# Optimization experiments

Measured on AMD Instinct MI355X. Metric: run time of the kernel, lower is better.

The kernel has to match this reference:

```python
import jax, jax.numpy as jnp
import numpy as np

B, M, N, F, H = 4, 512, 1024, 256, 256
K, K2, KC, RADIUS = 8, 4, 16, 0.5
EPS = 1e-5


def _cdist(a, b):
    d2 = (jnp.sum(a * a, -1)[..., :, None] + jnp.sum(b * b, -1)[..., None, :]
          - 2.0 * jnp.einsum('bnd,bmd->bnm', a, b))
    return jnp.sqrt(jnp.maximum(d2, 0.0))


def _scf_oe(xyz):
    # spherical coords (r, theta, phi) relative to cloud centroid -> (B,3,Npts)
    rel = xyz - jnp.mean(xyz, axis=1, keepdims=True)
    r = jnp.sqrt(jnp.sum(rel * rel, -1) + 1e-8)
    theta = jnp.arccos(jnp.clip(rel[..., 2] / r, -1.0, 1.0))
    phi = jnp.arctan2(rel[..., 1], rel[..., 0])
    return jnp.stack([r, theta, phi], axis=1)


def _knn_desc(xyz):
    # per-point SCF descriptor: sorted distances to KC nearest neighbors
    d = _cdist(xyz, xyz)
    return jnp.sort(d, axis=-1)[..., 1:KC + 1]


def _inorm(x):
    # InstanceNorm1d, affine=False: normalize over last dim per (b, row)
    mu = jnp.mean(x, -1, keepdims=True)
    var = jnp.var(x, -1, keepdims=True)
    return (x - mu) / jnp.sqrt(var + EPS)


def _conv1x1(x, W, g, b):
    # Conv2d 1x1 + BN(affine) + ReLU on (B,C,N,K)
    y = jnp.einsum('bcnk,oc->bonk', x, W)
    return jax.nn.relu(g[:, None, None] * y + b[:, None, None])


def _conv12(x, W, g, b):
    # Conv2d kernel (1,2) stride (1,2) + BN(affine) + ReLU on (B,C,N,P)
    Bb, C, Nn, P = x.shape
    xr = x.reshape(Bb, C, Nn, P // 2, 2)
    y = jnp.einsum('bcnpt,oct->bonp', xr, W)
    return jax.nn.relu(g[:, None, None] * y + b[:, None, None])


def _pointsift(xyz, feat, params):
    # PointSIFT OE: nearest neighbor in each of 8 octants within radius
    w1, g1, b1, w2, g2, b2, w3, g3, b3 = params
    Bb, Nn, _ = xyz.shape
    diff = xyz[:, None, :, :] - xyz[:, :, None, :]  # diff[b,i,j] = xyz[j]-xyz[i]
    d2 = jnp.sum(diff * diff, -1)
    octant = ((diff[..., 0] > 0).astype(jnp.int32) * 4
              + (diff[..., 1] > 0).astype(jnp.int32) * 2
              + (diff[..., 2] > 0).astype(jnp.int32))
    base = jnp.broadcast_to(jnp.arange(Nn)[None, :], (Bb, Nn))
    idxs = []
    for c in range(8):  # fixed small structural loop
        m = (octant == c) & (d2 <= RADIUS * RADIUS) & (d2 > 0)
        dm = jnp.where(m, d2, jnp.inf)
        j = jnp.argmin(dm, -1)
        valid = jnp.isfinite(jnp.min(dm, -1))
        idxs.append(jnp.where(valid, j, base))
    idx = jnp.stack(idxs, -1)  # (B,N,8)
    gxyz = jax.vmap(lambda p, i: p[i])(xyz, idx) - xyz[:, :, None, :]
    gfeat = jax.vmap(lambda f, i: f[i])(feat, idx)
    g = jnp.concatenate([gxyz, gfeat], -1).transpose(0, 3, 1, 2)  # (B,3+C,N,8)
    g = _conv12(g, w1, g1, b1)
    g = _conv12(g, w2, g2, b2)
    g = _conv12(g, w3, g3, b3)
    return g[..., 0]  # (B,C,N)


def setup_inputs():
    key = jax.random.key(0)
    ks = iter(jax.random.split(key, 64))
    rn = lambda shape, s=0.05: jax.random.normal(next(ks), shape, dtype=jnp.float32) * s
    ones = lambda shape: jnp.ones(shape, jnp.float32)
    zeros = lambda shape: jnp.zeros(shape, jnp.float32)
    inp = {
        'template_feature': rn((B, F, M), 1.0),
        'search_feature': rn((B, F, N), 1.0),
        'template_xyz': rn((B, M, 3), 1.0),
        'search_xyz': rn((B, N, 3), 1.0),
        'template_bc': rn((B, M, 9), 1.0),
        'search_bc': rn((B, N, 9), 1.0),
        'mlp_w1': rn((H, F + 3)), 'mlp_g1': ones(H), 'mlp_b1': zeros(H),
        'mlp_w2': rn((H, H)), 'mlp_g2': ones(H), 'mlp_b2': zeros(H),
        'mlp_w3': rn((H, H)), 'mlp_g3': ones(H), 'mlp_b3': zeros(H),
        'fea_w1': rn((F, H)), 'fea_g1': ones(F), 'fea_b1': zeros(F),
        'fea_w2': rn((F, F)), 'fea_bias2': zeros(F),
        'attn_wqkv': rn((3 * F, F)),
        'pos_w1': rn((64, 12)), 'pos_b1': zeros(64),
        'pos_w2': rn((F, 64)), 'pos_b2': zeros(F),
        'amlp_w1': rn((4 * F, F)), 'amlp_b1': zeros(4 * F),
        'amlp_w2': rn((F, 4 * F)), 'amlp_b2': zeros(F),
        'oe1_w1': rn((F, F + 3, 2)), 'oe1_g1': ones(F), 'oe1_b1': zeros(F),
        'oe1_w2': rn((F, F, 2)), 'oe1_g2': ones(F), 'oe1_b2': zeros(F),
        'oe1_w3': rn((F, F, 2)), 'oe1_g3': ones(F), 'oe1_b3': zeros(F),
        'oe2_w1': rn((F, F + 3, 2)), 'oe2_g1': ones(F), 'oe2_b1': zeros(F),
        'oe2_w2': rn((F, F, 2)), 'oe2_g2': ones(F), 'oe2_b2': zeros(F),
        'oe2_w3': rn((F, F, 2)), 'oe2_g3': ones(F), 'oe2_b3': zeros(F),
    }
    return inp


def reference(template_feature, search_feature, template_xyz, search_xyz, template_bc, search_bc,
              mlp_w1, mlp_g1, mlp_b1, mlp_w2, mlp_g2, mlp_b2, mlp_w3, mlp_g3, mlp_b3,
              fea_w1, fea_g1, fea_b1, fea_w2, fea_bias2,
              attn_wqkv, pos_w1, pos_b1, pos_w2, pos_b2, amlp_w1, amlp_b1, amlp_w2, amlp_b2,
              oe1_w1, oe1_g1, oe1_b1, oe1_w2, oe1_g2, oe1_b2, oe1_w3, oe1_g3, oe1_b3,
              oe2_w1, oe2_g1, oe2_b1, oe2_w2, oe2_g2, oe2_b2, oe2_w3, oe2_g3, oe2_b3):
    # ---- box-cloud distance + candidate pruning ----
    dist_bc = _cdist(template_bc, search_bc)  # (B,M,N)
    t_box = jnp.concatenate([template_xyz.transpose(0, 2, 1), template_bc.transpose(0, 2, 1),
                             template_feature, _scf_oe(template_xyz)], 1)  # (B,15+F,M)
    s_box = jnp.concatenate([search_xyz.transpose(0, 2, 1), search_bc.transpose(0, 2, 1),
                             search_feature, _scf_oe(search_xyz)], 1)      # (B,15+F,N)
    idx_b = jnp.argsort(dist_bc, axis=1)[:, :3 * K, :].transpose(0, 2, 1)  # (B,N,3K)
    dist_xyz = _cdist(search_xyz, template_xyz)  # (B,N,M)
    bi = jnp.arange(B)[:, None, None]
    ni = jnp.arange(N)[None, :, None]
    mask = jnp.full((B, N, M), 1e5, jnp.float32).at[bi, ni, idx_b].set(1.0)
    idx_k = jnp.argsort((dist_xyz * mask).transpose(0, 2, 1), axis=1)[:, :K, :].transpose(0, 2, 1)  # (B,N,K)
    # ---- SCF descriptor matching restricted to xyz candidates ----
    sd = _knn_desc(search_xyz)
    td = _knn_desc(template_xyz)
    mask2 = jnp.full((B, N, M), 1e5, jnp.float32).at[bi, ni, idx_k].set(1.0)
    dist_scf = _cdist(sd, td) * mask2
    idx_s = jnp.argsort(dist_scf.transpose(0, 2, 1), axis=1)[:, :K2, :].transpose(0, 2, 1)  # (B,N,K2)
    # ---- grouping + shared MLP ----
    corr = jax.vmap(lambda f, i: f[:, i])(t_box, idx_s)        # (B,15+F,N,K2)
    fused = jnp.concatenate([s_box[..., None], corr], -1)      # (B,15+F,N,K2+1)
    feats = fused.transpose(0, 2, 3, 1)[..., 12:]              # drop xyz+bc -> (B,N,K2+1,F+3)
    h = feats.transpose(0, 3, 1, 2)
    h = _conv1x1(h, mlp_w1, mlp_g1, mlp_b1)
    h = _conv1x1(h, mlp_w2, mlp_g2, mlp_b2)
    h = _conv1x1(h, mlp_w3, mlp_g3, mlp_b3)
    h = h.transpose(0, 2, 3, 1)                                # (B,N,K2+1,H)
    nn_xyz = corr[:, 0:3].transpose(0, 2, 3, 1)
    st_xyz = jnp.concatenate([search_xyz[:, :, None, :], nn_xyz], 2)
    nn_bc = corr[:, 3:12].transpose(0, 2, 3, 1)
    st_bc = jnp.concatenate([search_bc[:, :, None, :], nn_bc], 2)
    pos = jnp.concatenate([st_xyz, st_bc], -1)                 # (B,N,K2+1,12)
    KP1 = K2 + 1
    x = h.reshape(B * N, KP1, H)
    p = pos.reshape(B * N, KP1, 12)
    # ---- point transformer layer over tiny neighborhoods ----
    qkv = jnp.einsum('bnd,ed->bne', x, attn_wqkv)
    q, k, v = jnp.split(qkv, 3, axis=-1)
    rel_pos = p[:, :, None, :] - p[:, None, :, :]
    pe = jnp.einsum('bijp,hp->bijh', rel_pos, pos_w1) + pos_b1
    pe = jnp.einsum('bijh,dh->bijd', jax.nn.relu(pe), pos_w2) + pos_b2
    sim_in = q[:, :, None, :] - k[:, None, :, :] + pe
    hh = jax.nn.relu(jnp.einsum('bijd,hd->bijh', sim_in, amlp_w1) + amlp_b1)
    sim = jnp.einsum('bijh,dh->bijd', hh, amlp_w2) + amlp_b2
    attn = jax.nn.softmax(sim, axis=-2)
    agg = jnp.einsum('bijd,bijd->bid', attn, v[:, None, :, :] + pe)
    ff = agg.reshape(B, N, KP1, H).transpose(0, 3, 1, 2)[..., 0]  # (B,F,N)
    # ---- residual + instance norms + fea_layer ----
    ff = ff + search_feature
    ff = _inorm(ff.transpose(0, 2, 1)).transpose(0, 2, 1)
    y = jax.nn.relu(fea_g1[:, None] * jnp.einsum('bcn,oc->bon', ff, fea_w1) + fea_b1[:, None])
    y = jnp.einsum('bcn,oc->bon', y, fea_w2) + fea_bias2[:, None]
    y = _inorm((y + ff).transpose(0, 2, 1)).transpose(0, 2, 1)
    # ---- two PointSIFT OE modules with residuals ----
    y = y + _pointsift(search_xyz, y.transpose(0, 2, 1), (oe1_w1, oe1_g1, oe1_b1, oe1_w2, oe1_g2, oe1_b2, oe1_w3, oe1_g3, oe1_b3))
    y = y + _pointsift(search_xyz, y.transpose(0, 2, 1), (oe2_w1, oe2_g1, oe2_b1, oe2_w2, oe2_g2, oe2_b2, oe2_w3, oe2_g3, oe2_b3))
    return y
```

## Files before the change

### kernel.cpp

```cpp
#include <hip/hip_runtime.h>
#include <hip/hip_bf16.h>
#include <math.h>

constexpr int Bc = 4, Mc = 512, Nc = 1024, Fc = 256;
constexpr int KCc = 16;
constexpr float INFF = 3.0e38f;

typedef __attribute__((ext_vector_type(8))) short short8b;
typedef __attribute__((ext_vector_type(4))) float f32x4;

__device__ __forceinline__ short f2bf(float f) {
  __hip_bfloat16 h = __float2bfloat16(f);
  return *reinterpret_cast<short*>(&h);
}
__device__ __forceinline__ float bf2f(short s) {
  unsigned int u = ((unsigned int)(unsigned short)s) << 16;
  return __uint_as_float(u);
}
__device__ __forceinline__ unsigned long long umin64(unsigned long long a, unsigned long long b) {
  return a < b ? a : b;
}

__device__ __forceinline__ float blk_sum(float v, float* red) {
  int t = threadIdx.x;
// ... 34 lines not shown
    v = (k < 256) ? s.p[5][(size_t)(512 + r) * 256 + k] : pw2[(size_t)r * 64 + (k - 256)];
  else
    v = (k < K) ? s.p[job][(size_t)r * K + k] : 0.f;
  dstbase[gi] = f2bf(v);
}

__global__ __launch_bounds__(256) void scf_kernel(const float* __restrict__ xyz,
                                                  float* __restrict__ out, int P) {
  __shared__ float red[256];
  int b = blockIdx.x;
  const float* x = xyz + (size_t)b * P * 3;
  float sx = 0.f, sy = 0.f, sz = 0.f;
  for (int i = threadIdx.x; i < P; i += 256) {
    sx += x[3 * i]; sy += x[3 * i + 1]; sz += x[3 * i + 2];
  }
  float mx = blk_sum(sx, red) / (float)P;
  float my = blk_sum(sy, red) / (float)P;
  float mz = blk_sum(sz, red) / (float)P;
  for (int i = threadIdx.x; i < P; i += 256) {
    float a = x[3 * i] - mx, c = x[3 * i + 1] - my, d = x[3 * i + 2] - mz;
    float r = sqrtf(a * a + c * c + d * d + 1e-8f);
    float ct = d / r;
    ct = fminf(1.f, fmaxf(-1.f, ct));
    out[((size_t)b * 3 + 0) * P + i] = r;
    out[((size_t)b * 3 + 1) * P + i] = acosf(ct);
    out[((size_t)b * 3 + 2) * P + i] = atan2f(c, a);
  }
}

template <int P>
__global__ __launch_bounds__(256) void knn_kernel(const float* __restrict__ xyz,
                                                  float* __restrict__ desc) {
  constexpr int E = P / 64;
  int wv = threadIdx.x >> 6, l = threadIdx.x & 63;
  int pt = blockIdx.x * 4 + wv;
  int b = pt / P, i = pt % P;
  const float* x = xyz + (size_t)b * P * 3;
  float xi0 = x[3 * i], xi1 = x[3 * i + 1], xi2 = x[3 * i + 2];
  float d2r[E];
#pragma unroll
  for (int q = 0; q < E; ++q) {
    int j = q * 64 + l;
    float dx = x[3 * j] - xi0, dy = x[3 * j + 1] - xi1, dz = x[3 * j + 2] - xi2;
    d2r[q] = dx * dx + dy * dy + dz * dz;
  }
  for (int round = 0; round < KCc + 1; ++round) {
    unsigned long long k = ~0ULL;
#pragma unroll
    for (int q = 0; q < E; ++q) {
      unsigned long long c =
          ((unsigned long long)__float_as_uint(d2r[q]) << 32) | (unsigned)(q * 64 + l);
      k = umin64(k, c);
    }
#pragma unroll
    for (int m = 1; m < 64; m <<= 1) k = umin64(k, __shfl_xor(k, m));
    int widx = (int)(unsigned)k;
    if (round > 0 && l == 0)
      desc[((size_t)b * P + i) * KCc + (round - 1)] = sqrtf(__uint_as_float((unsigned)(k >> 32)));
    if ((widx & 63) == l) {
      int q = widx >> 6;
#pragma unroll
      for (int qq = 0; qq < E; ++qq)
        if (qq == q) d2r[qq] = INFF;
    }
  }
}

__global__ __launch_bounds__(256) void select_kernel(
    const float* __restrict__ tbc, const float* __restrict__ sbc,
    const float* __restrict__ txyz, const float* __restrict__ sxyz,
    const float* __restrict__ sd, const float* __restrict__ td,
    int* __restrict__ idx_s) {
  __shared__ int cand4[4][24];
  int wv = threadIdx.x >> 6, l = threadIdx.x & 63;
  int pt = blockIdx.x * 4 + wv;
  int b = pt / Nc, n = pt % Nc;
  const float* sb = sbc + ((size_t)b * Nc + n) * 9;
  float sreg[9];
#pragma unroll
  for (int c = 0; c < 9; ++c) sreg[c] = sb[c];
  float d2r[8];
#pragma unroll
  for (int q = 0; q < 8; ++q) {
    int m = q * 64 + l;
    const float* tb = tbc + ((size_t)b * Mc + m) * 9;
    float acc = 0.f;
#pragma unroll
    for (int c = 0; c < 9; ++c) { float d = tb[c] - sreg[c]; acc += d * d; }
    d2r[q] = acc;
  }
  for (int round = 0; round < 24; ++round) {
    unsigned long long k = ~0ULL;
#pragma unroll
    for (int q = 0; q < 8; ++q) {
      unsigned long long c =
          ((unsigned long long)__float_as_uint(d2r[q]) << 32) | (unsigned)(q * 64 + l);
      k = umin64(k, c);
    }
#pragma unroll
    for (int m = 1; m < 64; m <<= 1) k = umin64(k, __shfl_xor(k, m));
    int widx = (int)(unsigned)k;
    if (l == 0) cand4[wv][round] = widx;
    if ((widx & 63) == l) {
      int q = widx >> 6;
#pragma unroll
      for (int qq = 0; qq < 8; ++qq)
        if (qq == q) d2r[qq] = INFF;
    }
  }
  if (l == 0) {
    int* cand = cand4[wv];
    const float* sp = sxyz + ((size_t)b * Nc + n) * 3;
    float sx = sp[0], sy = sp[1], sz = sp[2];
    float dv[24];
    for (int t2 = 0; t2 < 24; ++t2) {
      const float* tp = txyz + ((size_t)b * Mc + cand[t2]) * 3;
      float dx = tp[0] - sx, dy = tp[1] - sy, dz = tp[2] - sz;
      dv[t2] = dx * dx + dy * dy + dz * dz;
    }
    int c8[8]; bool used[24];
    for (int t2 = 0; t2 < 24; ++t2) used[t2] = false;
    for (int r = 0; r < 8; ++r) {
      float bv = INFF; int bt = -1, bm = 0x7fffffff;
      for (int t2 = 0; t2 < 24; ++t2) {
        if (used[t2]) continue;
        int m = cand[t2];
        if (bt < 0 || dv[t2] < bv || (dv[t2] == bv && m < bm)) { bv = dv[t2]; bt = t2; bm = m; }
      }
      used[bt] = true; c8[r] = bm;
    }
    const float* sdp = sd + ((size_t)b * Nc + n) * KCc;
    float sdr[16];
    for (int t2 = 0; t2 < 16; ++t2) sdr[t2] = sdp[t2];
    float dscf[8];
    for (int r = 0; r < 8; ++r) {
      const float* tdp = td + ((size_t)b * Mc + c8[r]) * KCc;
      float acc = 0.f;
      for (int t2 = 0; t2 < 16; ++t2) { float d = sdr[t2] - tdp[t2]; acc += d * d; }
      dscf[r] = acc;
    }
    bool u8[8] = {false, false, false, false, false, false, false, false};
    for (int r = 0; r < 4; ++r) {
      float bv = INFF; int bt = -1, bm = 0x7fffffff;
      for (int t2 = 0; t2 < 8; ++t2) {
        if (u8[t2]) continue;
        if (bt < 0 || dscf[t2] < bv || (dscf[t2] == bv && c8[t2] < bm)) { bv = dscf[t2]; bt = t2; bm = c8[t2]; }
      }
      u8[bt] = true;
      idx_s[(((size_t)b * Nc + n) << 2) + r] = bm;
    }
  }
}

__global__ __launch_bounds__(512, 4) void mlp_kernel(
    const float* __restrict__ sfeat, const float* __restrict__ tfeat,
    const float* __restrict__ sscf, const float* __restrict__ tscf,
    const int* __restrict__ idx_s,
    const short* __restrict__ w1f, const float* __restrict__ g1, const float* __restrict__ b1,
    const short* __restrict__ w2f, const float* __restrict__ g2, const float* __restrict__ b2,
    const short* __restrict__ w3f, const float* __restrict__ g3, const float* __restrict__ b3,
    short* __restrict__ houtS) {
  __shared__ __align__(16) char smem[52224];
  char* B1 = smem;
  char* B2 = smem + 27648;
  char* B3 = smem;
  __shared__ int ms[32];
  int t = threadIdx.x;
  int tau0 = blockIdx.x * 8;
  int b = tau0 / Nc, n0 = tau0 % Nc;
  int h = t >> 8, ch = t & 255;
  if (t < 32) ms[t] = idx_s[(((size_t)b * Nc + n0 + (t >> 2)) << 2) + (t & 3)];
  __syncthreads();
  for (int z = t; z < 48 * 29; z += 512) {
    int col = z / 29, k = 259 + z % 29;
    *(short*)(B1 + ((col * 576 + 2 * k) ^ ((col & 7) << 4))) = 0;
  }
  for (int z = t; z < 8 * 259; z += 512) {
    int col = 40 + z / 259, k = z % 259;
    *(short*)(B1 + ((col * 576 + 2 * k) ^ ((col & 7) << 4))) = 0;
  }
  for (int sj = h; sj < 40; sj += 2) {
    int s = sj / 5, j = sj % 5;
    int n = n0 + s;
    int cx = (sj & 7) << 4;
    if (j == 0) {
      *(short*)(B1 + ((sj * 576 + 2 * ch) ^ cx)) = f2bf(sfeat[((size_t)b * Fc + ch) * Nc + n]);
      if (ch < 3)
        *(short*)(B1 + ((sj * 576 + (256 + ch) * 2) ^ cx)) = f2bf(sscf[((size_t)b * 3 + ch) * Nc + n]);
    } else {
      int m = ms[s * 4 + j - 1];
      *(short*)(B1 + ((sj * 576 + 2 * ch) ^ cx)) = f2bf(tfeat[((size_t)b * Fc + ch) * Mc + m]);
      if (ch < 3)
        *(short*)(B1 + ((sj * 576 + (256 + ch) * 2) ^ cx)) = f2bf(tscf[((size_t)b * 3 + ch) * Mc + m]);
    }
  }
  __syncthreads();
  int l = t & 63, w = t >> 6, lg = l >> 4, lr = l & 15;
  {
    f32x4 acc[2][3];
#pragma unroll
    for (int i = 0; i < 2; ++i)
#pragma unroll
      for (int ct = 0; ct < 3; ++ct) acc[i][ct] = (f32x4){0,0,0,0};
    for (int kk = 0; kk < 9; ++kk) {
      short8b bb[3];
#pragma unroll
      for (int ct = 0; ct < 3; ++ct) {
        int col = ct * 16 + lr;
        bb[ct] = *(const short8b*)(B1 + ((col * 576 + kk * 64 + lg * 16) ^ ((col & 7) << 4)));
      }
#pragma unroll
      for (int i = 0; i < 2; ++i) {
        short8b a = *(const short8b*)(w1f + (((size_t)((w * 2 + i) * 9 + kk)) * 64 + l) * 8);
#pragma unroll
        for (int ct = 0; ct < 3; ++ct)
          acc[i][ct] = __builtin_amdgcn_mfma_f32_16x16x32_bf16(a, bb[ct], acc[i][ct], 0, 0, 0);
      }
    }
    __syncthreads();
#pragma unroll
    for (int i = 0; i < 2; ++i) {
      int r0 = (w * 2 + i) * 16 + lg * 4;
      float4 gg = *(const float4*)(g1 + r0), bs = *(const float4*)(b1 + r0);
#pragma unroll
      for (int ct = 0; ct < 3; ++ct) {
        int col = ct * 16 + lr; int cx = (col & 7) << 4;
        ushort4 hv;
        hv.x = (unsigned short)f2bf(fmaxf(gg.x * acc[i][ct][0] + bs.x, 0.f));
        hv.y = (unsigned short)f2bf(fmaxf(gg.y * acc[i][ct][1] + bs.y, 0.f));
        hv.z = (unsigned short)f2bf(fmaxf(gg.z * acc[i][ct][2] + bs.z, 0.f));
        hv.w = (unsigned short)f2bf(fmaxf(gg.w * acc[i][ct][3] + bs.w, 0.f));
        *(ushort4*)(B2 + ((col * 512 + r0 * 2) ^ cx)) = hv;
      }
    }
  }
  __syncthreads();
  {
    f32x4 acc[2][3];
#pragma unroll
    for (int i = 0; i < 2; ++i)
#pragma unroll
      for (int ct = 0; ct < 3; ++ct) acc[i][ct] = (f32x4){0,0,0,0};
    for (int kk = 0; kk < 8; ++kk) {
      short8b bb[3];
#pragma unroll
      for (int ct = 0; ct < 3; ++ct) {
        int col = ct * 16 + lr;
        bb[ct] = *(const short8b*)(B2 + ((col * 512 + kk * 64 + lg * 16) ^ ((col & 7) << 4)));
      }
#pragma unroll
      for (int i = 0; i < 2; ++i) {
        short8b a = *(const short8b*)(w2f + (((size_t)((w * 2 + i) * 8 + kk)) * 64 + l) * 8);
#pragma unroll
        for (int ct = 0; ct < 3; ++ct)
          acc[i][ct] = __builtin_amdgcn_mfma_f32_16x16x32_bf16(a, bb[ct], acc[i][ct], 0, 0, 0);
      }
    }
    __syncthreads();
#pragma unroll
    for (int i = 0; i < 2; ++i) {
      int r0 = (w * 2 + i) * 16 + lg * 4;
      float4 gg = *(const float4*)(g2 + r0), bs = *(const float4*)(b2 + r0);
#pragma unroll
      for (int ct = 0; ct < 3; ++ct) {
        int col = ct * 16 + lr; int cx = (col & 7) << 4;
        ushort4 hv;
        hv.x = (unsigned short)f2bf(fmaxf(gg.x * acc[i][ct][0] + bs.x, 0.f));
        hv.y = (unsigned short)f2bf(fmaxf(gg.y * acc[i][ct][1] + bs.y, 0.f));
        hv.z = (unsigned short)f2bf(fmaxf(gg.z * acc[i][ct][2] + bs.z, 0.f));
        hv.w = (unsigned short)f2bf(fmaxf(gg.w * acc[i][ct][3] + bs.w, 0.f));
        *(ushort4*)(B3 + ((col * 512 + r0 * 2) ^ cx)) = hv;
      }
    }
  }
  __syncthreads();
  {
    f32x4 acc[2][3];
#pragma unroll
    for (int i = 0; i < 2; ++i)
#pragma unroll
      for (int ct = 0; ct < 3; ++ct) acc[i][ct] = (f32x4){0,0,0,0};
    for (int kk = 0; kk < 8; ++kk) {
      short8b bb[3];
#pragma unroll
      for (int ct = 0; ct < 3; ++ct) {
        int col = ct * 16 + lr;
        bb[ct] = *(const short8b*)(B3 + ((col * 512 + kk * 64 + lg * 16) ^ ((col & 7) << 4)));
      }
#pragma unroll
      for (int i = 0; i < 2; ++i) {
        short8b a = *(const short8b*)(w3f + (((size_t)((w * 2 + i) * 8 + kk)) * 64 + l) * 8);
#pragma unroll
        for (int ct = 0; ct < 3; ++ct)
          acc[i][ct] = __builtin_amdgcn_mfma_f32_16x16x32_bf16(a, bb[ct], acc[i][ct], 0, 0, 0);
      }
    }
#pragma unroll
    for (int i = 0; i < 2; ++i) {
      int r0 = (w * 2 + i) * 16 + lg * 4;
      float4 gg = *(const float4*)(g3 + r0), bs = *(const float4*)(b3 + r0);
#pragma unroll
      for (int ct = 0; ct < 3; ++ct) {
        int col = ct * 16 + lr;
        if (col < 40) {
          ushort4 hv;
          hv.x = (unsigned short)f2bf(fmaxf(gg.x * acc[i][ct][0] + bs.x, 0.f));
          hv.y = (unsigned short)f2bf(fmaxf(gg.y * acc[i][ct][1] + bs.y, 0.f));
          hv.z = (unsigned short)f2bf(fmaxf(gg.z * acc[i][ct][2] + bs.z, 0.f));
          hv.w = (unsigned short)f2bf(fmaxf(gg.w * acc[i][ct][3] + bs.w, 0.f));
          int s = col / 5, j = col % 5;
          *(ushort4*)(houtS + ((size_t)(tau0 + s) * 5 + j) * 256 + r0) = hv;
        }
      }
    }
  }
}

__global__ __launch_bounds__(512, 4) void attn_kernel(
    const short* __restrict__ hbufS, const int* __restrict__ idx_s,
    const float* __restrict__ sxyz, const float* __restrict__ sbc,
    const float* __restrict__ txyz, const float* __restrict__ tbc,
    const short* __restrict__ aqf, const short* __restrict__ akpef, const short* __restrict__ avpef,
    const float* __restrict__ pw1, const float* __restrict__ pb1, const float* __restrict__ pb2,
    const short* __restrict__ aw1f, const float* __restrict__ ab1,
    const short* __restrict__ aw2f, const float* __restrict__ ab2,
    const float* __restrict__ sfeat,
    const short* __restrict__ fw1f, const float* __restrict__ fg1, const float* __restrict__ fb1,
    const short* __restrict__ fw2f, const float* __restrict__ fb2v,
    float* __restrict__ yout) {
  __shared__ __align__(16) char smem[79872];
  char* Bx   = smem;
  char* vpeB = smem;
  char* feaB = smem;
  char* feaH = smem + 8192;
  float* y2F = (float*)(smem + 16384);
  char* KB   = smem + 30720;
  char* simS = smem + 30720;
  char* HpB  = smem + 55296;
  float* qF  = (float*)(smem + 55296);
  float* q04 = (float*)(smem + 55296);
  float* redf = (float*)(smem + 63488);
  float* pc4 = (float*)(smem + 64000);
  int t = threadIdx.x;
  int tau0 = blockIdx.x * 8;
  int b = tau0 / Nc, n0 = tau0 % Nc;
  int w = t >> 6, l = t & 63, lg = l >> 4, lr = l & 15;
  int h = t >> 8, ch = t & 255;
  for (int z = t; z < 2560; z += 512) {
    int col = 40 + z / 320, k = z % 320;
    *(short*)(Bx + ((col * 640 + 2 * k) ^ ((col & 7) << 4))) = 0;
  }
  for (int sj = h; sj < 40; sj += 2) {
    int s = sj / 5, j = sj % 5;
    *(short*)(Bx + ((sj * 640 + 2 * ch) ^ ((sj & 7) << 4))) =
        hbufS[(size_t)(tau0 + s) * 1280 + j * 256 + ch];
  }
  if (t < 40) {
    int s = t / 5, k = t % 5;
    int n = n0 + s;
    float* pd = pc4 + t * 12;
    if (k == 0) {
      for (int c = 0; c < 3; ++c) pd[c] = sxyz[((size_t)b * Nc + n) * 3 + c];
      for (int c = 0; c < 9; ++c) pd[3 + c] = sbc[((size_t)b * Nc + n) * 9 + c];
    } else {
      int m = idx_s[(((size_t)b * Nc + n) << 2) + (k - 1)];
      for (int c = 0; c < 3; ++c) pd[c] = txyz[((size_t)b * Mc + m) * 3 + c];
      for (int c = 0; c < 9; ++c) pd[3 + c] = tbc[((size_t)b * Mc + m) * 9 + c];
    }
  }
  __syncthreads();
  for (int it = t; it < 2560; it += 512) {
    int sj = it >> 6, hh = it & 63;
    int s = sj / 5;
    float acc = pb1[hh];
    const float* wv = pw1 + hh * 12;
    const float* p0 = pc4 + (s * 5) * 12;
    const float* pj = pc4 + sj * 12;
#pragma unroll
    for (int p = 0; p < 12; ++p) acc += wv[p] * (p0[p] - pj[p]);
    *(short*)(Bx + ((sj * 640 + 512 + 2 * hh) ^ ((sj & 7) << 4))) = f2bf(fmaxf(acc, 0.f));
  }
  __syncthreads();
  {
    f32x4 qA[2][3];
#pragma unroll
    for (int i = 0; i < 2; ++i)
#pragma unroll
      for (int ct = 0; ct < 3; ++ct) qA[i][ct] = (f32x4){0,0,0,0};
    for (int kk = 0; kk < 8; ++kk) {
      short8b bq[3];
#pragma unroll
      for (int ct = 0; ct < 3; ++ct) {
        int col = ct * 16 + lr;
        bq[ct] = *(const short8b*)(Bx + ((col * 640 + kk * 64 + lg * 16) ^ ((col & 7) << 4)));
      }
#pragma unroll
      for (int i = 0; i < 2; ++i) {
        short8b a = *(const short8b*)(aqf + (((size_t)((w * 2 + i) * 8 + kk)) * 64 + l) * 8);
#pragma unroll
        for (int ct = 0; ct < 3; ++ct)
          qA[i][ct] = __builtin_amdgcn_mfma_f32_16x16x32_bf16(a, bq[ct], qA[i][ct], 0, 0, 0);
      }
    }
#pragma unroll
    for (int i = 0; i < 2; ++i) {
      int r0 = (w * 2 + i) * 16 + lg * 4;
#pragma unroll
      for (int ct = 0; ct < 3; ++ct) {
        int col = ct * 16 + lr;
        if (col < 40 && col % 5 == 0)
          *(f32x4*)(qF + (col / 5) * 256 + r0) = qA[i][ct];
      }
    }
  }
  f32x4 sA[2][3], vA[2][3];
#pragma unroll
  for (int i = 0; i < 2; ++i)
#pragma unroll
    for (int ct = 0; ct < 3; ++ct) { sA[i][ct] = (f32x4){0,0,0,0}; vA[i][ct] = (f32x4){0,0,0,0}; }
  for (int kk = 0; kk < 10; ++kk) {
    short8b bb[3];
#pragma unroll
    for (int ct = 0; ct < 3; ++ct) {
      int col = ct * 16 + lr;
      bb[ct] = *(const short8b*)(Bx + ((col * 640 + kk * 64 + lg * 16) ^ ((col & 7) << 4)));
    }
#pragma unroll
    for (int i = 0; i < 2; ++i) {
      short8b ak = *(const short8b*)(akpef + (((size_t)((w * 2 + i) * 10 + kk)) * 64 + l) * 8);
      short8b av = *(const short8b*)(avpef + (((size_t)((w * 2 + i) * 10 + kk)) * 64 + l) * 8);
#pragma unroll
      for (int ct = 0; ct < 3; ++ct) {
        sA[i][ct] = __builtin_amdgcn_mfma_f32_16x16x32_bf16(ak, bb[ct], sA[i][ct], 0, 0, 0);
        vA[i][ct] = __builtin_amdgcn_mfma_f32_16x16x32_bf16(av, bb[ct], vA[i][ct], 0, 0, 0);
      }
    }
  }
  __syncthreads();
#pragma unroll
  for (int i = 0; i < 2; ++i) {
    int r0 = (w * 2 + i) * 16 + lg * 4;
    float4 pb = *(const float4*)(pb2 + r0);
#pragma unroll
    for (int ct = 0; ct < 3; ++ct) {
      int col = ct * 16 + lr; int cx = (col & 7) << 4;
      if (col < 40) {
        int s = col / 5;
        f32x4 qv = *(const f32x4*)(qF + s * 256 + r0);
        ushort4 kv, vv;
        kv.x = (unsigned short)f2bf(qv[0] + sA[i][ct][0] + pb.x);
        kv.y = (unsigned short)f2bf(qv[1] + sA[i][ct][1] + pb.y);
        kv.z = (unsigned short)f2bf(qv[2] + sA[i][ct][2] + pb.z);
        kv.w = (unsigned short)f2bf(qv[3] + sA[i][ct][3] + pb.w);
        vv.x = (unsigned short)f2bf(vA[i][ct][0] + pb.x);
        vv.y = (unsigned short)f2bf(vA[i][ct][1] + pb.y);
        vv.z = (unsigned short)f2bf(vA[i][ct][2] + pb.z);
        vv.w = (unsigned short)f2bf(vA[i][ct][3] + pb.w);
        *(ushort4*)(KB + ((col * 512 + r0 * 2) ^ cx)) = kv;
        *(ushort4*)(vpeB + ((col * 512 + r0 * 2) ^ cx)) = vv;
      } else {
        ushort4 zz; zz.x = zz.y = zz.z = zz.w = 0;
        *(ushort4*)(KB + ((col * 512 + r0 * 2) ^ cx)) = zz;
      }
    }
  }
  __syncthreads();
  f32x4 sacc[2][3];
#pragma unroll
  for (int i = 0; i < 2; ++i)
#pragma unroll
    for (int ct = 0; ct < 3; ++ct) sacc[i][ct] = (f32x4){0,0,0,0};
  for (int p = 0; p < 4; ++p) {
    f32x4 hacc[2][3];
#pragma unroll
    for (int i = 0; i < 2; ++i)
#pragma unroll
      for (int ct = 0; ct < 3; ++ct) hacc[i][ct] = (f32x4){0,0,0,0};
    for (int kk = 0; kk < 8; ++kk) {
      short8b bb[3];
#pragma unroll
      for (int ct = 0; ct < 3; ++ct) {
        int col = ct * 16 + lr;
        bb[ct] = *(const short8b*)(KB + ((col * 512 + kk * 64 + lg * 16) ^ ((col & 7) << 4)));
      }
#pragma unroll
      for (int i = 0; i < 2; ++i) {
        int rtg = p * 16 + w * 2 + i;
        short8b a = *(const short8b*)(aw1f + (((size_t)(rtg * 8 + kk)) * 64 + l) * 8);
#pragma unroll
        for (int ct = 0; ct < 3; ++ct)
          hacc[i][ct] = __builtin_amdgcn_mfma_f32_16x16x32_bf16(a, bb[ct], hacc[i][ct], 0, 0, 0);
      }
    }
#pragma unroll
    for (int i = 0; i < 2; ++i) {
      int r0l = (w * 2 + i) * 16 + lg * 4;
      float4 bias = *(const float4*)(ab1 + p * 256 + r0l);
#pragma unroll
      for (int ct = 0; ct < 3; ++ct) {
        int col = ct * 16 + lr; int cx = (col & 7) << 4;
        ushort4 hv;
        hv.x = (unsigned short)f2bf(fmaxf(hacc[i][ct][0] + bias.x, 0.f));
        hv.y = (unsigned short)f2bf(fmaxf(hacc[i][ct][1] + bias.y, 0.f));
        hv.z = (unsigned short)f2bf(fmaxf(hacc[i][ct][2] + bias.z, 0.f));
        hv.w = (unsigned short)f2bf(fmaxf(hacc[i][ct][3] + bias.w, 0.f));
        *(ushort4*)(HpB + ((col * 512 + r0l * 2) ^ cx)) = hv;
      }
    }
    __syncthreads();
// ... 291 lines not shown
        *(short*)(B2 + ((col2 * 1024 + (2 * (r0 + 1) + tp) * 2) ^ cx2)) =
            f2bf(fmaxf(gg.y * acc[i][ct][1] + bs.y, 0.f));
        *(short*)(B2 + ((col2 * 1024 + (2 * (r0 + 2) + tp) * 2) ^ cx2)) =
            f2bf(fmaxf(gg.z * acc[i][ct][2] + bs.z, 0.f));
        *(short*)(B2 + ((col2 * 1024 + (2 * (r0 + 3) + tp) * 2) ^ cx2)) =
            f2bf(fmaxf(gg.w * acc[i][ct][3] + bs.w, 0.f));
      }
    }
  }
  __syncthreads();
  {
    f32x4 acc[2];
#pragma unroll
    for (int i = 0; i < 2; ++i) acc[i] = (f32x4){0,0,0,0};
    for (int kk = 0; kk < 16; ++kk) {
      short8b b0 = *(const short8b*)(B2 + ((lr * 1024 + kk * 64 + lg * 16) ^ ((lr & 7) << 4)));
#pragma unroll
      for (int i = 0; i < 2; ++i) {
        short8b a = *(const short8b*)(w2f + (((size_t)((w * 2 + i) * 16 + kk)) * 64 + l) * 8);
        acc[i] = __builtin_amdgcn_mfma_f32_16x16x32_bf16(a, b0, acc[i], 0, 0, 0);
      }
    }
    __syncthreads();
    int s = lr >> 1, tp = lr & 1;
    int col3 = s; int cx3 = (col3 & 7) << 4;
#pragma unroll
    for (int i = 0; i < 2; ++i) {
      int r0 = (w * 2 + i) * 16 + lg * 4;
      float4 gg = *(const float4*)(g2 + r0), bs = *(const float4*)(b2 + r0);
      *(short*)(B3 + ((col3 * 1024 + (2 * r0 + tp) * 2) ^ cx3)) =
          f2bf(fmaxf(gg.x * acc[i][0] + bs.x, 0.f));
      *(short*)(B3 + ((col3 * 1024 + (2 * (r0 + 1) + tp) * 2) ^ cx3)) =
          f2bf(fmaxf(gg.y * acc[i][1] + bs.y, 0.f));
      *(short*)(B3 + ((col3 * 1024 + (2 * (r0 + 2) + tp) * 2) ^ cx3)) =
          f2bf(fmaxf(gg.z * acc[i][2] + bs.z, 0.f));
      *(short*)(B3 + ((col3 * 1024 + (2 * (r0 + 3) + tp) * 2) ^ cx3)) =
          f2bf(fmaxf(gg.w * acc[i][3] + bs.w, 0.f));
    }
  }
  __syncthreads();
  {
    f32x4 acc[2];
#pragma unroll
    for (int i = 0; i < 2; ++i) acc[i] = (f32x4){0,0,0,0};
    for (int kk = 0; kk < 16; ++kk) {
      short8b b0 = *(const short8b*)(B3 + ((lr * 1024 + kk * 64 + lg * 16) ^ ((lr & 7) << 4)));
#pragma unroll
      for (int i = 0; i < 2; ++i) {
        short8b a = *(const short8b*)(w3f + (((size_t)((w * 2 + i) * 16 + kk)) * 64 + l) * 8);
        acc[i] = __builtin_amdgcn_mfma_f32_16x16x32_bf16(a, b0, acc[i], 0, 0, 0);
      }
    }
#pragma unroll
    for (int i = 0; i < 2; ++i) {
      if (lr < 8) {
        int s = lr;
        int r0 = (w * 2 + i) * 16 + lg * 4;
        float4 gg = *(const float4*)(g3 + r0), bs = *(const float4*)(b3 + r0);
        float4 yv = *(const float4*)(yin + ((size_t)(i0 + s)) * 256 + r0);
        float4 ov;
        ov.x = yv.x + fmaxf(gg.x * acc[i][0] + bs.x, 0.f);
        ov.y = yv.y + fmaxf(gg.y * acc[i][1] + bs.y, 0.f);
        ov.z = yv.z + fmaxf(gg.z * acc[i][2] + bs.z, 0.f);
        ov.w = yv.w + fmaxf(gg.w * acc[i][3] + bs.w, 0.f);
        *(float4*)(yout + ((size_t)(i0 + s)) * 256 + r0) = ov;
      }
    }
  }
}

__global__ __launch_bounds__(256) void transpose_kernel(const float* __restrict__ yin,
                                                        float* __restrict__ out) {
  __shared__ float tile[64][65];
  int bid = blockIdx.x;
  int b = bid >> 6;
  int tl = bid & 63;
  int n0 = (tl >> 2) * 64;
  int c0 = (tl & 3) * 64;
  int tx = threadIdx.x & 63, ty = threadIdx.x >> 6;
#pragma unroll
  for (int r = 0; r < 16; ++r) {
    int i = r * 4 + ty;
    tile[i][tx] = yin[((size_t)b * Nc + n0 + i) * 256 + c0 + tx];
  }
  __syncthreads();
#pragma unroll
  for (int r = 0; r < 16; ++r) {
    int j = r * 4 + ty;
    out[((size_t)b * Fc + c0 + j) * Nc + n0 + tx] = tile[tx][j];
  }
}

extern "C" void kernel_launch(void* const* d_in, const int* in_sizes, int n_in,
                              void* d_out, int out_size, void* d_ws, size_t ws_size,
                              hipStream_t stream) {
  (void)in_sizes; (void)n_in; (void)out_size; (void)ws_size;
  const float* tfeat = (const float*)d_in[0];
  const float* sfeat = (const float*)d_in[1];
  const float* txyz  = (const float*)d_in[2];
  const float* sxyz  = (const float*)d_in[3];
  const float* tbc   = (const float*)d_in[4];
  const float* sbc   = (const float*)d_in[5];
  const float* mw1 = (const float*)d_in[6];
  const float* mg1 = (const float*)d_in[7];
  const float* mb1 = (const float*)d_in[8];
  const float* mw2 = (const float*)d_in[9];
  const float* mg2 = (const float*)d_in[10];
  const float* mb2 = (const float*)d_in[11];
  const float* mw3 = (const float*)d_in[12];
  const float* mg3 = (const float*)d_in[13];
  const float* mb3 = (const float*)d_in[14];
  const float* fw1 = (const float*)d_in[15];
  const float* fg1 = (const float*)d_in[16];
  const float* fb1 = (const float*)d_in[17];
  const float* fw2 = (const float*)d_in[18];
  const float* fb2 = (const float*)d_in[19];
  const float* wqkv = (const float*)d_in[20];
  const float* pw1 = (const float*)d_in[21];
  const float* pb1 = (const float*)d_in[22];
  const float* pw2 = (const float*)d_in[23];
  const float* pb2 = (const float*)d_in[24];
  const float* aw1 = (const float*)d_in[25];
  const float* ab1 = (const float*)d_in[26];
  const float* aw2 = (const float*)d_in[27];
  const float* ab2 = (const float*)d_in[28];
  const float* o1w1 = (const float*)d_in[29];
  const float* o1g1 = (const float*)d_in[30];
  const float* o1b1 = (const float*)d_in[31];
  const float* o1w2 = (const float*)d_in[32];
  const float* o1g2 = (const float*)d_in[33];
  const float* o1b2 = (const float*)d_in[34];
  const float* o1w3 = (const float*)d_in[35];
  const float* o1g3 = (const float*)d_in[36];
  const float* o1b3 = (const float*)d_in[37];
  const float* o2w1 = (const float*)d_in[38];
  const float* o2g1 = (const float*)d_in[39];
  const float* o2b1 = (const float*)d_in[40];
  const float* o2w2 = (const float*)d_in[41];
  const float* o2g2 = (const float*)d_in[42];
  const float* o2b2 = (const float*)d_in[43];
  const float* o2w3 = (const float*)d_in[44];
  const float* o2g3 = (const float*)d_in[45];
  const float* o2b3 = (const float*)d_in[46];

  float* ws = (float*)d_ws;
  float* sd   = ws;
  float* td   = sd + 65536;
  float* sscf = td + 32768;
  float* tscf = sscf + 12288;
  int*   idxs = (int*)(tscf + 6144);
  int*   sidx = idxs + 16384;
  float* yws  = (float*)(sidx + 32768);
  short* sb   = (short*)(yws + 1048576);
  short* hbufS = sb;
  short* mw1f  = sb + 5242880;
  short* mw2f  = mw1f + 73728;
  short* mw3f  = mw2f + 65536;
  short* aqf   = mw3f + 65536;
  short* akpef = aqf + 65536;
  short* avpef = akpef + 81920;
  short* aw1f  = avpef + 81920;
  short* aw2f  = aw1f + 262144;
  short* fw1f  = aw2f + 262144;
  short* fw2f  = fw1f + 65536;
  short* o1w1f = fw2f + 65536;
  short* o1w2f = o1w1f + 139264;
  short* o1w3f = o1w2f + 131072;
  short* o2w1f = o1w3f + 131072;
  short* o2w2f = o2w1f + 139264;
  short* o2w3f = o2w2f + 131072;
  float* ybuf2 = (float*)sb;

  WSrcs srcs;
  srcs.p[0] = mw1;  srcs.p[1] = mw2;  srcs.p[2] = mw3;  srcs.p[3] = wqkv;
  srcs.p[4] = wqkv; srcs.p[5] = wqkv; srcs.p[6] = aw1;  srcs.p[7] = aw2;
  srcs.p[8] = fw1;  srcs.p[9] = fw2;  srcs.p[10] = o1w1; srcs.p[11] = o1w2;
  srcs.p[12] = o1w3; srcs.p[13] = o2w1; srcs.p[14] = o2w2; srcs.p[15] = o2w3;
  wconv_all<<<7392, 256, 0, stream>>>(srcs, pw2, mw1f);

  scf_kernel<<<Bc, 256, 0, stream>>>(sxyz, sscf, Nc);
  scf_kernel<<<Bc, 256, 0, stream>>>(txyz, tscf, Mc);
  knn_kernel<Nc><<<Bc * Nc / 4, 256, 0, stream>>>(sxyz, sd);
  knn_kernel<Mc><<<Bc * Mc / 4, 256, 0, stream>>>(txyz, td);
  select_kernel<<<Bc * Nc / 4, 256, 0, stream>>>(tbc, sbc, txyz, sxyz, sd, td, idxs);
  mlp_kernel<<<Bc * Nc / 8, 512, 0, stream>>>(sfeat, tfeat, sscf, tscf, idxs,
                                              mw1f, mg1, mb1, mw2f, mg2, mb2,
                                              mw3f, mg3, mb3, hbufS);
  attn_kernel<<<Bc * Nc / 8, 512, 0, stream>>>(hbufS, idxs, sxyz, sbc, txyz, tbc,
                                               aqf, akpef, avpef, pw1, pb1, pb2,
                                               aw1f, ab1, aw2f, ab2,
                                               sfeat, fw1f, fg1, fb1, fw2f, fb2, yws);
  sift_idx_kernel<<<Bc * Nc / 4, 256, 0, stream>>>(sxyz, sidx);
  sift_oe_kernel<<<Bc * Nc / 8, 512, 0, stream>>>(sxyz, sidx, yws,
                                                  o1w1f, o1g1, o1b1, o1w2f, o1g2, o1b2,
                                                  o1w3f, o1g3, o1b3, ybuf2);
  sift_oe_kernel<<<Bc * Nc / 8, 512, 0, stream>>>(sxyz, sidx, ybuf2,
                                                  o2w1f, o2g1, o2b1, o2w2f, o2g2, o2b2,
                                                  o2w3f, o2g3, o2b3, yws);
  transpose_kernel<<<256, 256, 0, stream>>>(yws, (float*)d_out);
}
```

Baseline: 315.9 us.

## Fuse MLP stage into attention kernel, keeping hidden features in LDS

Merges the three-layer MLP kernel into the attention kernel so the per-point hidden features go straight from the MLP epilogue into the attention input buffer in shared memory. This drops the global round-trip of the bf16 hidden buffer and one kernel launch. MLP buffers are placed in distinct LDS regions, with an extra barrier, so the final layer can write into the attention layout. The fused kernel keeps the larger 78KB LDS footprint for the whole run, which may limit occupancy during the MLP phase.

```diff
diff --git a/kernel.cpp b/kernel.cpp
--- a/kernel.cpp
+++ b/kernel.cpp
@@ -210,183 +210,26 @@
   }
 }
 
-__global__ __launch_bounds__(512, 4) void mlp_kernel(
+__global__ __launch_bounds__(512, 4) void mlp_attn_kernel(
     const float* __restrict__ sfeat, const float* __restrict__ tfeat,
     const float* __restrict__ sscf, const float* __restrict__ tscf,
     const int* __restrict__ idx_s,
-    const short* __restrict__ w1f, const float* __restrict__ g1, const float* __restrict__ b1,
-    const short* __restrict__ w2f, const float* __restrict__ g2, const float* __restrict__ b2,
-    const short* __restrict__ w3f, const float* __restrict__ g3, const float* __restrict__ b3,
-    short* __restrict__ houtS) {
-  __shared__ __align__(16) char smem[52224];
-  char* B1 = smem;
-  char* B2 = smem + 27648;
-  char* B3 = smem;
-  __shared__ int ms[32];
-  int t = threadIdx.x;
-  int tau0 = blockIdx.x * 8;
-  int b = tau0 / Nc, n0 = tau0 % Nc;
-  int h = t >> 8, ch = t & 255;
-  if (t < 32) ms[t] = idx_s[(((size_t)b * Nc + n0 + (t >> 2)) << 2) + (t & 3)];
-  __syncthreads();
-  for (int z = t; z < 48 * 29; z += 512) {
-    int col = z / 29, k = 259 + z % 29;
-    *(short*)(B1 + ((col * 576 + 2 * k) ^ ((col & 7) << 4))) = 0;
-  }
-  for (int z = t; z < 8 * 259; z += 512) {
-    int col = 40 + z / 259, k = z % 259;
-    *(short*)(B1 + ((col * 576 + 2 * k) ^ ((col & 7) << 4))) = 0;
-  }
-  for (int sj = h; sj < 40; sj += 2) {
-    int s = sj / 5, j = sj % 5;
-    int n = n0 + s;
-    int cx = (sj & 7) << 4;
-    if (j == 0) {
-      *(short*)(B1 + ((sj * 576 + 2 * ch) ^ cx)) = f2bf(sfeat[((size_t)b * Fc + ch) * Nc + n]);
-      if (ch < 3)
-        *(short*)(B1 + ((sj * 576 + (256 + ch) * 2) ^ cx)) = f2bf(sscf[((size_t)b * 3 + ch) * Nc + n]);
-    } else {
-      int m = ms[s * 4 + j - 1];
-      *(short*)(B1 + ((sj * 576 + 2 * ch) ^ cx)) = f2bf(tfeat[((size_t)b * Fc + ch) * Mc + m]);
-      if (ch < 3)
-        *(short*)(B1 + ((sj * 576 + (256 + ch) * 2) ^ cx)) = f2bf(tscf[((size_t)b * 3 + ch) * Mc + m]);
-    }
-  }
-  __syncthreads();
-  int l = t & 63, w = t >> 6, lg = l >> 4, lr = l & 15;
-  {
-    f32x4 acc[2][3];
-#pragma unroll
-    for (int i = 0; i < 2; ++i)
-#pragma unroll
-      for (int ct = 0; ct < 3; ++ct) acc[i][ct] = (f32x4){0,0,0,0};
-    for (int kk = 0; kk < 9; ++kk) {
-      short8b bb[3];
-#pragma unroll
-      for (int ct = 0; ct < 3; ++ct) {
-        int col = ct * 16 + lr;
-        bb[ct] = *(const short8b*)(B1 + ((col * 576 + kk * 64 + lg * 16) ^ ((col & 7) << 4)));
-      }
-#pragma unroll
-      for (int i = 0; i < 2; ++i) {
-        short8b a = *(const short8b*)(w1f + (((size_t)((w * 2 + i) * 9 + kk)) * 64 + l) * 8);
-#pragma unroll
-        for (int ct = 0; ct < 3; ++ct)
-          acc[i][ct] = __builtin_amdgcn_mfma_f32_16x16x32_bf16(a, bb[ct], acc[i][ct], 0, 0, 0);
-      }
-    }
-    __syncthreads();
-#pragma unroll
-    for (int i = 0; i < 2; ++i) {
-      int r0 = (w * 2 + i) * 16 + lg * 4;
-      float4 gg = *(const float4*)(g1 + r0), bs = *(const float4*)(b1 + r0);
-#pragma unroll
-      for (int ct = 0; ct < 3; ++ct) {
-        int col = ct * 16 + lr; int cx = (col & 7) << 4;
-        ushort4 hv;
-        hv.x = (unsigned short)f2bf(fmaxf(gg.x * acc[i][ct][0] + bs.x, 0.f));
-        hv.y = (unsigned short)f2bf(fmaxf(gg.y * acc[i][ct][1] + bs.y, 0.f));
-        hv.z = (unsigned short)f2bf(fmaxf(gg.z * acc[i][ct][2] + bs.z, 0.f));
-        hv.w = (unsigned short)f2bf(fmaxf(gg.w * acc[i][ct][3] + bs.w, 0.f));
-        *(ushort4*)(B2 + ((col * 512 + r0 * 2) ^ cx)) = hv;
-      }
-    }
-  }
-  __syncthreads();
-  {
-    f32x4 acc[2][3];
-#pragma unroll
-    for (int i = 0; i < 2; ++i)
-#pragma unroll
-      for (int ct = 0; ct < 3; ++ct) acc[i][ct] = (f32x4){0,0,0,0};
-    for (int kk = 0; kk < 8; ++kk) {
-      short8b bb[3];
-#pragma unroll
-      for (int ct = 0; ct < 3; ++ct) {
-        int col = ct * 16 + lr;
-        bb[ct] = *(const short8b*)(B2 + ((col * 512 + kk * 64 + lg * 16) ^ ((col & 7) << 4)));
-      }
-#pragma unroll
-      for (int i = 0; i < 2; ++i) {
-        short8b a = *(const short8b*)(w2f + (((size_t)((w * 2 + i) * 8 + kk)) * 64 + l) * 8);
-#pragma unroll
-        for (int ct = 0; ct < 3; ++ct)
-          acc[i][ct] = __builtin_amdgcn_mfma_f32_16x16x32_bf16(a, bb[ct], acc[i][ct], 0, 0, 0);
-      }
-    }
-    __syncthreads();
-#pragma unroll
-    for (int i = 0; i < 2; ++i) {
-      int r0 = (w * 2 + i) * 16 + lg * 4;
-      float4 gg = *(const float4*)(g2 + r0), bs = *(const float4*)(b2 + r0);
-#pragma unroll
-      for (int ct = 0; ct < 3; ++ct) {
-        int col = ct * 16 + lr; int cx = (col & 7) << 4;
-        ushort4 hv;
-        hv.x = (unsigned short)f2bf(fmaxf(gg.x * acc[i][ct][0] + bs.x, 0.f));
-        hv.y = (unsigned short)f2bf(fmaxf(gg.y * acc[i][ct][1] + bs.y, 0.f));
-        hv.z = (unsigned short)f2bf(fmaxf(gg.z * acc[i][ct][2] + bs.z, 0.f));
-        hv.w = (unsigned short)f2bf(fmaxf(gg.w * acc[i][ct][3] + bs.w, 0.f));
-        *(ushort4*)(B3 + ((col * 512 + r0 * 2) ^ cx)) = hv;
-      }
-    }
-  }
-  __syncthreads();
-  {
-    f32x4 acc[2][3];
-#pragma unroll
-    for (int i = 0; i < 2; ++i)
-#pragma unroll
-      for (int ct = 0; ct < 3; ++ct) acc[i][ct] = (f32x4){0,0,0,0};
-    for (int kk = 0; kk < 8; ++kk) {
-      short8b bb[3];
-#pragma unroll
-      for (int ct = 0; ct < 3; ++ct) {
-        int col = ct * 16 + lr;
-        bb[ct] = *(const short8b*)(B3 + ((col * 512 + kk * 64 + lg * 16) ^ ((col & 7) << 4)));
-      }
-#pragma unroll
-      for (int i = 0; i < 2; ++i) {
-        short8b a = *(const short8b*)(w3f + (((size_t)((w * 2 + i) * 8 + kk)) * 64 + l) * 8);
-#pragma unroll
-        for (int ct = 0; ct < 3; ++ct)
-          acc[i][ct] = __builtin_amdgcn_mfma_f32_16x16x32_bf16(a, bb[ct], acc[i][ct], 0, 0, 0);
-      }
-    }
-#pragma unroll
-    for (int i = 0; i < 2; ++i) {
-      int r0 = (w * 2 + i) * 16 + lg * 4;
-      float4 gg = *(const float4*)(g3 + r0), bs = *(const float4*)(b3 + r0);
-#pragma unroll
-      for (int ct = 0; ct < 3; ++ct) {
-        int col = ct * 16 + lr;
-        if (col < 40) {
-          ushort4 hv;
-          hv.x = (unsigned short)f2bf(fmaxf(gg.x * acc[i][ct][0] + bs.x, 0.f));
-          hv.y = (unsigned short)f2bf(fmaxf(gg.y * acc[i][ct][1] + bs.y, 0.f));
-          hv.z = (unsigned short)f2bf(fmaxf(gg.z * acc[i][ct][2] + bs.z, 0.f));
-          hv.w = (unsigned short)f2bf(fmaxf(gg.w * acc[i][ct][3] + bs.w, 0.f));
-          int s = col / 5, j = col % 5;
-          *(ushort4*)(houtS + ((size_t)(tau0 + s) * 5 + j) * 256 + r0) = hv;
-        }
-      }
-    }
-  }
-}
-
-__global__ __launch_bounds__(512, 4) void attn_kernel(
-    const short* __restrict__ hbufS, const int* __restrict__ idx_s,
+    const short* __restrict__ mw1f, const float* __restrict__ mg1, const float* __restrict__ mb1,
+    const short* __restrict__ mw2f, const float* __restrict__ mg2, const float* __restrict__ mb2,
+    const short* __restrict__ mw3f, const float* __restrict__ mg3, const float* __restrict__ mb3,
     const float* __restrict__ sxyz, const float* __restrict__ sbc,
     const float* __restrict__ txyz, const float* __restrict__ tbc,
     const short* __restrict__ aqf, const short* __restrict__ akpef, const short* __restrict__ avpef,
     const float* __restrict__ pw1, const float* __restrict__ pb1, const float* __restrict__ pb2,
     const short* __restrict__ aw1f, const float* __restrict__ ab1,
     const short* __restrict__ aw2f, const float* __restrict__ ab2,
-    const float* __restrict__ sfeat,
     const short* __restrict__ fw1f, const float* __restrict__ fg1, const float* __restrict__ fb1,
     const short* __restrict__ fw2f, const float* __restrict__ fb2v,
     float* __restrict__ yout) {
   __shared__ __align__(16) char smem[79872];
+  char* mB1 = smem;
+  char* mB2 = smem + 27648;
+  char* mB3 = smem + 52224;
   char* Bx   = smem;
   char* vpeB = smem;
   char* feaB = smem;
@@ -399,20 +242,162 @@
   float* q04 = (float*)(smem + 55296);
   float* redf = (float*)(smem + 63488);
   float* pc4 = (float*)(smem + 64000);
+  __shared__ int ms[32];
   int t = threadIdx.x;
   int tau0 = blockIdx.x * 8;
   int b = tau0 / Nc, n0 = tau0 % Nc;
   int w = t >> 6, l = t & 63, lg = l >> 4, lr = l & 15;
   int h = t >> 8, ch = t & 255;
-  for (int z = t; z < 2560; z += 512) {
-    int col = 40 + z / 320, k = z % 320;
-    *(short*)(Bx + ((col * 640 + 2 * k) ^ ((col & 7) << 4))) = 0;
+  if (t < 32) ms[t] = idx_s[(((size_t)b * Nc + n0 + (t >> 2)) << 2) + (t & 3)];
+  __syncthreads();
+  for (int z = t; z < 48 * 29; z += 512) {
+    int col = z / 29, k = 259 + z % 29;
+    *(short*)(mB1 + ((col * 576 + 2 * k) ^ ((col & 7) << 4))) = 0;
+  }
+  for (int z = t; z < 8 * 259; z += 512) {
+    int col = 40 + z / 259, k = z % 259;
+    *(short*)(mB1 + ((col * 576 + 2 * k) ^ ((col & 7) << 4))) = 0;
   }
   for (int sj = h; sj < 40; sj += 2) {
     int s = sj / 5, j = sj % 5;
-    *(short*)(Bx + ((sj * 640 + 2 * ch) ^ ((sj & 7) << 4))) =
-        hbufS[(size_t)(tau0 + s) * 1280 + j * 256 + ch];
-  }
+    int n = n0 + s;
+    int cx = (sj & 7) << 4;
+    if (j == 0) {
+      *(short*)(mB1 + ((sj * 576 + 2 * ch) ^ cx)) = f2bf(sfeat[((size_t)b * Fc + ch) * Nc + n]);
+      if (ch < 3)
+        *(short*)(mB1 + ((sj * 576 + (256 + ch) * 2) ^ cx)) = f2bf(sscf[((size_t)b * 3 + ch) * Nc + n]);
+    } else {
+      int m = ms[s * 4 + j - 1];
+      *(short*)(mB1 + ((sj * 576 + 2 * ch) ^ cx)) = f2bf(tfeat[((size_t)b * Fc + ch) * Mc + m]);
+      if (ch < 3)
+        *(short*)(mB1 + ((sj * 576 + (256 + ch) * 2) ^ cx)) = f2bf(tscf[((size_t)b * 3 + ch) * Mc + m]);
+    }
+  }
+  __syncthreads();
+  {
+    f32x4 acc[2][3];
+#pragma unroll
+    for (int i = 0; i < 2; ++i)
+#pragma unroll
+      for (int ct = 0; ct < 3; ++ct) acc[i][ct] = (f32x4){0,0,0,0};
+    for (int kk = 0; kk < 9; ++kk) {
+      short8b bb[3];
+#pragma unroll
+      for (int ct = 0; ct < 3; ++ct) {
+        int col = ct * 16 + lr;
+        bb[ct] = *(const short8b*)(mB1 + ((col * 576 + kk * 64 + lg * 16) ^ ((col & 7) << 4)));
+      }
+#pragma unroll
+      for (int i = 0; i < 2; ++i) {
+        short8b a = *(const short8b*)(mw1f + (((size_t)((w * 2 + i) * 9 + kk)) * 64 + l) * 8);
+#pragma unroll
+        for (int ct = 0; ct < 3; ++ct)
+          acc[i][ct] = __builtin_amdgcn_mfma_f32_16x16x32_bf16(a, bb[ct], acc[i][ct], 0, 0, 0);
+      }
+    }
+    __syncthreads();
+#pragma unroll
+    for (int i = 0; i < 2; ++i) {
+      int r0 = (w * 2 + i) * 16 + lg * 4;
+      float4 gg = *(const float4*)(mg1 + r0), bs = *(const float4*)(mb1 + r0);
+#pragma unroll
+      for (int ct = 0; ct < 3; ++ct) {
+        int col = ct * 16 + lr; int cx = (col & 7) << 4;
+        ushort4 hv;
+        hv.x = (unsigned short)f2bf(fmaxf(gg.x * acc[i][ct][0] + bs.x, 0.f));
+        hv.y = (unsigned short)f2bf(fmaxf(gg.y * acc[i][ct][1] + bs.y, 0.f));
+        hv.z = (unsigned short)f2bf(fmaxf(gg.z * acc[i][ct][2] + bs.z, 0.f));
+        hv.w = (unsigned short)f2bf(fmaxf(gg.w * acc[i][ct][3] + bs.w, 0.f));
+        *(ushort4*)(mB2 + ((col * 512 + r0 * 2) ^ cx)) = hv;
+      }
+    }
+  }
+  __syncthreads();
+  {
+    f32x4 acc[2][3];
+#pragma unroll
+    for (int i = 0; i < 2; ++i)
+#pragma unroll
+      for (int ct = 0; ct < 3; ++ct) acc[i][ct] = (f32x4){0,0,0,0};
+    for (int kk = 0; kk < 8; ++kk) {
+      short8b bb[3];
+#pragma unroll
+      for (int ct = 0; ct < 3; ++ct) {
+        int col = ct * 16 + lr;
+        bb[ct] = *(const short8b*)(mB2 + ((col * 512 + kk * 64 + lg * 16) ^ ((col & 7) << 4)));
+      }
+#pragma unroll
+      for (int i = 0; i < 2; ++i) {
+        short8b a = *(const short8b*)(mw2f + (((size_t)((w * 2 + i) * 8 + kk)) * 64 + l) * 8);
+#pragma unroll
+        for (int ct = 0; ct < 3; ++ct)
+          acc[i][ct] = __builtin_amdgcn_mfma_f32_16x16x32_bf16(a, bb[ct], acc[i][ct], 0, 0, 0);
+      }
+    }
+    __syncthreads();
+#pragma unroll
+    for (int i = 0; i < 2; ++i) {
+      int r0 = (w * 2 + i) * 16 + lg * 4;
+      float4 gg = *(const float4*)(mg2 + r0), bs = *(const float4*)(mb2 + r0);
+#pragma unroll
+      for (int ct = 0; ct < 3; ++ct) {
+        int col = ct * 16 + lr; int cx = (col & 7) << 4;
+        ushort4 hv;
+        hv.x = (unsigned short)f2bf(fmaxf(gg.x * acc[i][ct][0] + bs.x, 0.f));
+        hv.y = (unsigned short)f2bf(fmaxf(gg.y * acc[i][ct][1] + bs.y, 0.f));
+        hv.z = (unsigned short)f2bf(fmaxf(gg.z * acc[i][ct][2] + bs.z, 0.f));
+        hv.w = (unsigned short)f2bf(fmaxf(gg.w * acc[i][ct][3] + bs.w, 0.f));
+        *(ushort4*)(mB3 + ((col * 512 + r0 * 2) ^ cx)) = hv;
+      }
+    }
+  }
+  __syncthreads();
+  {
+    f32x4 acc[2][3];
+#pragma unroll
+    for (int i = 0; i < 2; ++i)
+#pragma unroll
+      for (int ct = 0; ct < 3; ++ct) acc[i][ct] = (f32x4){0,0,0,0};
+    for (int kk = 0; kk < 8; ++kk) {
+      short8b bb[3];
+#pragma unroll
+      for (int ct = 0; ct < 3; ++ct) {
+        int col = ct * 16 + lr;
+        bb[ct] = *(const short8b*)(mB3 + ((col * 512 + kk * 64 + lg * 16) ^ ((col & 7) << 4)));
+      }
+#pragma unroll
+      for (int i = 0; i < 2; ++i) {
+        short8b a = *(const short8b*)(mw3f + (((size_t)((w * 2 + i) * 8 + kk)) * 64 + l) * 8);
+#pragma unroll
+        for (int ct = 0; ct < 3; ++ct)
+          acc[i][ct] = __builtin_amdgcn_mfma_f32_16x16x32_bf16(a, bb[ct], acc[i][ct], 0, 0, 0);
+      }
+    }
+    __syncthreads();
+#pragma unroll
+    for (int i = 0; i < 2; ++i) {
+      int r0 = (w * 2 + i) * 16 + lg * 4;
+      float4 gg = *(const float4*)(mg3 + r0), bs = *(const float4*)(mb3 + r0);
+#pragma unroll
+      for (int ct = 0; ct < 3; ++ct) {
+        int col = ct * 16 + lr;
+        if (col < 40) {
+          int cx = (col & 7) << 4;
+          ushort4 hv;
+          hv.x = (unsigned short)f2bf(fmaxf(gg.x * acc[i][ct][0] + bs.x, 0.f));
+          hv.y = (unsigned short)f2bf(fmaxf(gg.y * acc[i][ct][1] + bs.y, 0.f));
+          hv.z = (unsigned short)f2bf(fmaxf(gg.z * acc[i][ct][2] + bs.z, 0.f));
+          hv.w = (unsigned short)f2bf(fmaxf(gg.w * acc[i][ct][3] + bs.w, 0.f));
+          *(ushort4*)(Bx + ((col * 640 + r0 * 2) ^ cx)) = hv;
+        }
+      }
+    }
+    for (int z = t; z < 2560; z += 512) {
+      int col = 40 + z / 320, k = z % 320;
+      *(short*)(Bx + ((col * 640 + 2 * k) ^ ((col & 7) << 4))) = 0;
+    }
+  }
+  __syncthreads();
   if (t < 40) {
     int s = t / 5, k = t % 5;
     int n = n0 + s;
@@ -1010,7 +995,6 @@
   int*   sidx = idxs + 16384;
   float* yws  = (float*)(sidx + 32768);
   short* sb   = (short*)(yws + 1048576);
-  short* hbufS = sb;
   short* mw1f  = sb + 5242880;
   short* mw2f  = mw1f + 73728;
   short* mw3f  = mw2f + 65536;
@@ -1041,13 +1025,13 @@
   knn_kernel<Nc><<<Bc * Nc / 4, 256, 0, stream>>>(sxyz, sd);
   knn_kernel<Mc><<<Bc * Mc / 4, 256, 0, stream>>>(txyz, td);
   select_kernel<<<Bc * Nc / 4, 256, 0, stream>>>(tbc, sbc, txyz, sxyz, sd, td, idxs);
-  mlp_kernel<<<Bc * Nc / 8, 512, 0, stream>>>(sfeat, tfeat, sscf, tscf, idxs,
-                                              mw1f, mg1, mb1, mw2f, mg2, mb2,
-                                              mw3f, mg3, mb3, hbufS);
-  attn_kernel<<<Bc * Nc / 8, 512, 0, stream>>>(hbufS, idxs, sxyz, sbc, txyz, tbc,
-                                               aqf, akpef, avpef, pw1, pb1, pb2,
-                                               aw1f, ab1, aw2f, ab2,
-                                               sfeat, fw1f, fg1, fb1, fw2f, fb2, yws);
+  mlp_attn_kernel<<<Bc * Nc / 8, 512, 0, stream>>>(
+      sfeat, tfeat, sscf, tscf, idxs,
+      mw1f, mg1, mb1, mw2f, mg2, mb2, mw3f, mg3, mb3,
+      sxyz, sbc, txyz, tbc,
+      aqf, akpef, avpef, pw1, pb1, pb2,
+      aw1f, ab1, aw2f, ab2,
+      fw1f, fg1, fb1, fw2f, fb2, yws);
   sift_idx_kernel<<<Bc * Nc / 4, 256, 0, stream>>>(sxyz, sidx);
   sift_oe_kernel<<<Bc * Nc / 8, 512, 0, stream>>>(sxyz, sidx, yws,
                                                   o1w1f, o1g1, o1b1, o1w2f, o1g2, o1b2,
```

New measurement: 315.4 us (median of 2 runs). No clear change (-0.2%).
